# Performance work log

Hardware: AMD Instinct MI355X
Metric: run time of the kernel (lower is better)

The kernel has to match this reference:

```python
import math
import jax, jax.numpy as jnp
import numpy as np

H = 12
D_MODEL = 768
D_K = D_MODEL // H
B, S = 2, 2048


def setup_inputs() -> dict:
    key = jax.random.key(0)
    ks = jax.random.split(key, 12)
    sc = 0.02
    inp = {
        "query": jax.random.normal(ks[0], (B, S, D_MODEL), jnp.float32),
        "key": jax.random.normal(ks[1], (B, S, D_MODEL), jnp.float32),
        "value": jax.random.normal(ks[2], (B, S, D_MODEL), jnp.float32),
        # causal mask [B, S, S]: 1 where attendable
        "mask": jnp.broadcast_to(jnp.tril(jnp.ones((S, S), jnp.int32)), (B, S, S)),
        "Wq": sc * jax.random.normal(ks[3], (D_MODEL, D_MODEL), jnp.float32),
        "bq": jnp.zeros((D_MODEL,), jnp.float32),
        "Wk": sc * jax.random.normal(ks[4], (D_MODEL, D_MODEL), jnp.float32),
        "bk": jnp.zeros((D_MODEL,), jnp.float32),
        "Wv": sc * jax.random.normal(ks[5], (D_MODEL, D_MODEL), jnp.float32),
        "bv": jnp.zeros((D_MODEL,), jnp.float32),
        "Wo": sc * jax.random.normal(ks[6], (D_MODEL, D_MODEL), jnp.float32),
        "bo": jnp.zeros((D_MODEL,), jnp.float32),
    }
    return inp


def reference(query, key, value, mask, Wq, bq, Wk, bk, Wv, bv, Wo, bo):
    b, s, _ = query.shape
    # linear projections (torch Linear: x @ W.T + b), split into heads
    def proj(x, W, bias):
        return (x @ W.T + bias).reshape(b, s, H, D_K).transpose(0, 2, 1, 3)  # [B,H,S,Dk]

    q = proj(query, Wq, bq)
    k = proj(key, Wk, bk)
    v = proj(value, Wv, bv)

    scores = jnp.einsum("bhqd,bhkd->bhqk", q, k) / math.sqrt(D_K)  # [B,H,S,S]
    # exponential time-decay bias over key positions 1..S, shape [1,1,1,S]
    time = jnp.exp(-jnp.arange(1, s + 1, dtype=scores.dtype))[None, None, None, :]
    scores = jnp.where(mask[:, None, :, :] == 0, jnp.asarray(-1e9, scores.dtype), scores)
    p_attn = jax.nn.softmax(scores - time, axis=-1)
    x = jnp.einsum("bhqk,bhkd->bhqd", p_attn, v)  # [B,H,S,Dk]
    x = x.transpose(0, 2, 1, 3).reshape(b, s, H * D_K)
    return x @ Wo.T + bo
```

## Files before the change

### kernel.cpp

```cpp
#include <hip/hip_runtime.h>
#include <hip/hip_bf16.h>
#include <math.h>

typedef __bf16 bf16;
typedef __attribute__((ext_vector_type(8))) __bf16 bf16x8;
typedef __attribute__((ext_vector_type(4))) __bf16 bf16x4;
typedef __attribute__((ext_vector_type(4))) float floatx4;
typedef __attribute__((ext_vector_type(16))) float floatx16;

#define NH 12
#define DK 64
#define DM 768
#define NB 2
#define SEQ 2048
#define MTOT (NB * SEQ)
#define WELEM (DM * DM)
#define XELEM (MTOT * DM)

#define QSCALE 0.1803368801111832f
#define LOG2E 1.4426950408889634f

static __device__ __forceinline__ bf16x8 load8(const bf16* p) {
    return *(const bf16x8*)p;
}
static __device__ __forceinline__ float4 ld4(const float* p) {
    return *(const float4*)p;
}
static __device__ __forceinline__ bf16x8 cvt8(const float4 a, const float4 b) {
    bf16x8 r;
    r[0] = (bf16)a.x; r[1] = (bf16)a.y; r[2] = (bf16)a.z; r[3] = (bf16)a.w;
    r[4] = (bf16)b.x; r[5] = (bf16)b.y; r[6] = (bf16)b.z; r[7] = (bf16)b.w;
    return r;
}
static __device__ __forceinline__ float fast_exp2(float x) {
#if __has_builtin(__builtin_amdgcn_exp2f)
    return __builtin_amdgcn_exp2f(x);
#else
    return __expf(x * 0.6931471805599453f);
#endif
}
static __device__ __forceinline__ floatx16 zero16() {
    floatx16 z;
#pragma unroll
    for (int i = 0; i < 16; i++) z[i] = 0.f;
    return z;
}
static __device__ __forceinline__ void async16(const bf16* g, bf16* l) {
    __builtin_amdgcn_global_load_lds((const __attribute__((address_space(1))) void*)g,
                                     (__attribute__((address_space(3))) void*)l,
                                     16, 0, 0);
}

__global__ __launch_bounds__(256) void cvt_kernel(
    const float* __restrict__ wq, const float* __restrict__ wk,
    const float* __restrict__ wv, const float* __restrict__ wo,
    const float* __restrict__ xq, const float* __restrict__ xk, const float* __restrict__ xv,
    bf16* __restrict__ Wb, bf16* __restrict__ Wob,
    bf16* __restrict__ Xqb, bf16* __restrict__ Xkb, bf16* __restrict__ Xvb) {
    const int g = blockIdx.x * 256 + threadIdx.x;
    const int PW = WELEM / 8;
    const int PX = XELEM / 8;
    if (g < 4 * PW) {
        const int wi = g / PW;
        const int rem = g - wi * PW;
        const int n = rem / 96;
        const int t = rem - n * 96;
        const int s = t >> 3;
        const int j = t & 7;
        const float* src = (wi == 0) ? wq : (wi == 1) ? wk : (wi == 2) ? wv : wo;
        bf16* dst = (wi < 3) ? (Wb + (size_t)wi * WELEM) : Wob;
        const float* p = src + (size_t)n * DM + s * 64 + j * 8;
        *(bf16x8*)(dst + (size_t)n * DM + s * 64 + ((j ^ (n & 7)) * 8)) = cvt8(ld4(p), ld4(p + 4));
    } else {
        const int gx = g - 4 * PW;
        const int xi = gx / PX;
        const int rem = gx - xi * PX;
        const int m = rem / 96;
        const int t = rem - m * 96;
        const int s = t >> 3;
        const int j = t & 7;
        const float* src = (xi == 0) ? xq : (xi == 1) ? xk : xv;
        bf16* dst = (xi == 0) ? Xqb : (xi == 1) ? Xkb : Xvb;
        const float* p = src + (size_t)m * DM + s * 64 + j * 8;
        *(bf16x8*)(dst + (size_t)m * DM + s * 64 + ((j ^ (m & 7)) * 8)) = cvt8(ld4(p), ld4(p + 4));
    }
}

__global__ __launch_bounds__(256, 3) void qkv_kernel(
    const bf16* __restrict__ Xqb, const bf16* __restrict__ Xkb, const bf16* __restrict__ Xvb,
    const bf16* __restrict__ Wb,
    const float* __restrict__ bq, const float* __restrict__ bk, const float* __restrict__ bv,
    bf16* __restrict__ Oq, bf16* __restrict__ Ok, bf16* __restrict__ Ov) {
    __shared__ __align__(16) bf16 SM[2 * 64 * 64 + 2 * 128 * 64];
    bf16* As0 = SM;
    bf16* Bs0 = SM + 8192;

    const int tid = threadIdx.x;
    const int id = blockIdx.x;
    const int xcd = id & 7;
    const int sl = id >> 3;
    const int z = sl / 48;
    const int r = sl % 48;
    const int m0 = (xcd * 8 + r / 6) * 64;
    const int n0 = (r % 6) * 128;

    const bf16* X = (z == 0) ? Xqb : (z == 1) ? Xkb : Xvb;
    const bf16* W = Wb + (size_t)z * WELEM;
    const float* bias = (z == 0) ? bq : (z == 1) ? bk : bv;
    bf16* out = (z == 0) ? Oq : (z == 1) ? Ok : Ov;

    const int wv = tid >> 6;
    const int wm = wv >> 1, wn = wv & 1;
    const int lane = tid & 63;
    const int ln = lane & 15;
    const int kq = lane >> 4;
    const int drow = lane >> 3;
    const int dcol = (lane & 7) * 8;

    floatx4 acc[2][4];
#pragma unroll
    for (int i = 0; i < 2; i++)
#pragma unroll
        for (int j = 0; j < 4; j++) acc[i][j] = (floatx4){0.f, 0.f, 0.f, 0.f};

#pragma unroll
    for (int it = 0; it < 2; it++)
        async16(X + (size_t)(m0 + wv * 16 + it * 8 + drow) * DM + dcol,
                As0 + (wv * 16 + it * 8) * 64);
#pragma unroll
    for (int it = 0; it < 4; it++)
        async16(W + (size_t)(n0 + wv * 32 + it * 8 + drow) * DM + dcol,
                Bs0 + (wv * 32 + it * 8) * 64);

    for (int k = 0; k < 12; k++) {
        __syncthreads();
        const bf16* Ap = As0 + (k & 1) * 4096;
        const bf16* Bp = Bs0 + (k & 1) * 8192;
        if (k < 11) {
            const int kc = (k + 1) * 64;
            bf16* An = As0 + ((k + 1) & 1) * 4096;
            bf16* Bn = Bs0 + ((k + 1) & 1) * 8192;
#pragma unroll
            for (int it = 0; it < 2; it++)
                async16(X + (size_t)(m0 + wv * 16 + it * 8 + drow) * DM + kc + dcol,
                        An + (wv * 16 + it * 8) * 64);
#pragma unroll
            for (int it = 0; it < 4; it++)
                async16(W + (size_t)(n0 + wv * 32 + it * 8 + drow) * DM + kc + dcol,
                        Bn + (wv * 32 + it * 8) * 64);
        }
#pragma unroll
        for (int ks = 0; ks < 2; ks++) {
            const int jb = (ks * 4 + kq) ^ (ln & 7);
            bf16x8 af[2], bfm[4];
#pragma unroll
            for (int mt = 0; mt < 2; mt++)
                af[mt] = *(const bf16x8*)&Ap[(wm * 32 + mt * 16 + ln) * 64 + jb * 8];
#pragma unroll
            for (int nt = 0; nt < 4; nt++)
                bfm[nt] = *(const bf16x8*)&Bp[(wn * 64 + nt * 16 + ln) * 64 + jb * 8];
#pragma unroll
            for (int mt = 0; mt < 2; mt++)
#pragma unroll
                for (int nt = 0; nt < 4; nt++)
                    acc[mt][nt] = __builtin_amdgcn_mfma_f32_16x16x32_bf16(af[mt], bfm[nt], acc[mt][nt], 0, 0, 0);
        }
    }

    float bv4[4];
#pragma unroll
    for (int nt = 0; nt < 4; nt++) bv4[nt] = bias[n0 + wn * 64 + nt * 16 + ln];

    if (z < 2) {
        const float qs = (z == 0) ? QSCALE : 1.0f;
        __syncthreads();
        bf16 (*E)[136] = (bf16(*)[136])SM;
#pragma unroll
        for (int mt = 0; mt < 2; mt++)
#pragma unroll
            for (int nt = 0; nt < 4; nt++)
#pragma unroll
                for (int r2 = 0; r2 < 4; r2++)
                    E[wm * 32 + mt * 16 + kq * 4 + r2][wn * 64 + nt * 16 + ln] =
                        (bf16)((acc[mt][nt][r2] + bv4[nt]) * qs);
        __syncthreads();
        const int row = tid >> 2;
        const int cb = (tid & 3) * 32;
        const int m = m0 + row;
        const int b = m >> 11;
        const int s = m & (SEQ - 1);
        const int h = (n0 + cb) >> 6;
        const int d = (n0 + cb) & 63;
        bf16* op = &out[((size_t)(b * NH + h) * SEQ + s) * DK + d];
#pragma unroll
        for (int q2 = 0; q2 < 4; q2++)
            *(bf16x8*)(op + q2 * 8) = *(bf16x8*)&E[row][cb + q2 * 8];
    } else {
        __syncthreads();
        bf16 (*E)[72] = (bf16(*)[72])SM;
#pragma unroll
        for (int nt = 0; nt < 4; nt++)
#pragma unroll
            for (int mt = 0; mt < 2; mt++) {
                bf16x4 v;
#pragma unroll
                for (int r2 = 0; r2 < 4; r2++) v[r2] = (bf16)(acc[mt][nt][r2] + bv4[nt]);
                *(bf16x4*)&E[wn * 64 + nt * 16 + ln][wm * 32 + mt * 16 + kq * 4] = v;
            }
        __syncthreads();
        const int row = tid >> 1;
        const int sc = (tid & 1) * 32;
        const int b = m0 >> 11;
        const int s0 = m0 & (SEQ - 1);
        const int h = (n0 >> 6) + (row >> 6);
        const int d = row & 63;
        bf16* op = &out[(size_t)(b * NH + h) * DK * SEQ + (size_t)d * SEQ + s0 + sc];
#pragma unroll
        for (int q2 = 0; q2 < 4; q2++)
            *(bf16x8*)(op + q2 * 8) = *(bf16x8*)&E[row][sc + q2 * 8];
    }
}


#define PERMK(r) (((r) & ~12) | (((r) & 4) << 1) | (((r) & 8) >> 1))
#define VSWZ(g, d) (((g) & 8) | (((g) & 7) ^ ((d) & 7)))

#define STAGE(kc)                                                                   \
    {                                                                               \
        bf16* kb_ = SM + group * 16384;                                             \
        bf16* vb_ = kb_ + 8192;                                                     \
        const int kk0 = (kc) * 128;                                                 \
        _Pragma("unroll")                                                           \
        for (int it = 0; it < 4; it++) {                                            \
            const int sk = qw * 4 + it;                                             \
            const int rK = sk * 8 + (lane >> 3);                                    \
            const int jbK = lane & 7;                                               \
            async16(Kb + (size_t)(kk0 + PERMK(rK)) * DK + ((jbK ^ (rK & 7)) * 8),   \
                    kb_ + sk * 512);                                                \
            const int dV = sk * 4 + (lane >> 4);                                    \
            const int jbV = lane & 15;                                              \
            async16(Vb + (size_t)dV * SEQ + kk0 + (VSWZ(jbV, dV) * 8),              \
                    vb_ + sk * 512);                                                \
        }                                                                           \
    }

#define CHUNK_BODY(FIRSTC)                                                          \
    _Pragma("unroll")                                                               \
    for (int c2 = 0; c2 < 4; c2++) {                                                \
        const int rowk = c2 * 32 + ln32;                                            \
        const bf16* krow = Kc + rowk * 64;                                          \
        const int rs = rowk & 7;                                                    \
        const bf16x8 a0 = *(const bf16x8*)&krow[((0 + hi) ^ rs) * 8];               \
        const bf16x8 a1 = *(const bf16x8*)&krow[((2 + hi) ^ rs) * 8];               \
        const bf16x8 a2 = *(const bf16x8*)&krow[((4 + hi) ^ rs) * 8];               \
        const bf16x8 a3 = *(const bf16x8*)&krow[((6 + hi) ^ rs) * 8];               \
        floatx16 t = zero16();                                                      \
        __builtin_amdgcn_s_setprio(1);                                              \
        t = __builtin_amdgcn_mfma_f32_32x32x16_bf16(a0, qb0, t, 0, 0, 0);           \
        t = __builtin_amdgcn_mfma_f32_32x32x16_bf16(a1, qb1, t, 0, 0, 0);           \
        t = __builtin_amdgcn_mfma_f32_32x32x16_bf16(a2, qb2, t, 0, 0, 0);           \
        t = __builtin_amdgcn_mfma_f32_32x32x16_bf16(a3, qb3, t, 0, 0, 0);           \
        __builtin_amdgcn_s_setprio(0);                                              \
        bf16x8 pa0, pa1;                                                            \
        _Pragma("unroll")                                                           \
        for (int r = 0; r < 16; r++) {                                              \
            const int kg = k0 + c2 * 32 + ((r >> 3) << 4) + (hi << 3) + (r & 7);    \
            float sv = t[r];                                                        \
            if (FIRSTC) sv -= __expf(-(float)(kg + 1)) * LOG2E;                     \
            float pf = fast_exp2(sv);                                               \
            if (lastc && kg > qgl) pf = 0.f;                                        \
            lsum += pf;                                                             \
            if (r < 8) pa0[r] = (bf16)pf; else pa1[r & 7] = (bf16)pf;               \
        }                                                                           \
        __builtin_amdgcn_s_setprio(1);                                              \
        {                                                                           \
            const bf16* v0 = Vc + ln32 * 128;                                       \
            const bf16* v1 = Vc + (32 + ln32) * 128;                                \
            const int ds = ln32 & 7;                                                \
            bf16x8 vb;                                                              \
            vb = *(const bf16x8*)&v0[VSWZ(c2 * 4 + hi, ds) * 8];                    \
            Oacc0 = __builtin_amdgcn_mfma_f32_32x32x16_bf16(pa0, vb, Oacc0, 0, 0, 0); \
            vb = *(const bf16x8*)&v0[VSWZ(c2 * 4 + 2 + hi, ds) * 8];                \
            Oacc0 = __builtin_amdgcn_mfma_f32_32x32x16_bf16(pa1, vb, Oacc0, 0, 0, 0); \
            vb = *(const bf16x8*)&v1[VSWZ(c2 * 4 + hi, ds) * 8];                    \
            Oacc1 = __builtin_amdgcn_mfma_f32_32x32x16_bf16(pa0, vb, Oacc1, 0, 0, 0); \
            vb = *(const bf16x8*)&v1[VSWZ(c2 * 4 + 2 + hi, ds) * 8];                \
            Oacc1 = __builtin_amdgcn_mfma_f32_32x32x16_bf16(pa1, vb, Oacc1, 0, 0, 0); \
        }                                                                           \
        __builtin_amdgcn_s_setprio(0);                                              \
    }

__global__ __launch_bounds__(512) void attn_kernel(const bf16* __restrict__ Q,
                                                   const bf16* __restrict__ K,
                                                   const bf16* __restrict__ Vt,
                                                   bf16* __restrict__ Xout) {
    __shared__ __align__(16) bf16 SM[2 * 16384];

    const int tid = threadIdx.x;
    const int gw = tid >> 6;
    const int group = gw >> 2;
    const int qw = gw & 3;
    const int lane = tid & 63;
    const int ln32 = lane & 31;
    const int hi = lane >> 5;

    const int b0 = blockIdx.x;
    const int t = (b0 < 192) ? (15 - b0 / 24) : ((b0 - 192) / 24);
    const int bh = b0 % 24;

    const int q0 = t * 128;
    const int nch = t + 1;

    const bf16* Qb = Q + (size_t)bh * SEQ * DK;
    const bf16* Kb = K + (size_t)bh * SEQ * DK;
    const bf16* Vb = Vt + (size_t)bh * SEQ * DK;

    const int qrow = q0 + qw * 32 + ln32;
    const int qgl = qrow;

    const bf16x8 qb0 = load8(Qb + (size_t)qrow * DK + 0 + hi * 8);
    const bf16x8 qb1 = load8(Qb + (size_t)qrow * DK + 16 + hi * 8);
    const bf16x8 qb2 = load8(Qb + (size_t)qrow * DK + 32 + hi * 8);
    const bf16x8 qb3 = load8(Qb + (size_t)qrow * DK + 48 + hi * 8);

    float lsum = 0.f;
    floatx16 Oacc0 = zero16(), Oacc1 = zero16();

    const int R = (nch + 1) >> 1;
    for (int r = 0; r < R; r++) {
        const int c = 2 * r + group;
        const bool active = (c < nch);
        __syncthreads();
        if (active) STAGE(c)
        asm volatile("s_waitcnt vmcnt(0)" ::: "memory");
        __syncthreads();
        if (active) {
            const int k0 = c * 128;
            const bool lastc = (c == nch - 1);
            const bf16* Kc = SM + group * 16384;
            const bf16* Vc = Kc + 8192;
            if (c == 0) {
                CHUNK_BODY(true)
            } else {
                CHUNK_BODY(false)
            }
        }
    }

    lsum += __shfl_xor(lsum, 32, 64);

    __syncthreads();
    float* LF = (float*)SM;
    float* LS = (float*)SM + 128 * 68;
    if (group == 1) {
#pragma unroll
        for (int r = 0; r < 16; r++) {
            const int rq = (r & 3) + ((r >> 2) << 3) + (hi << 2);
            LF[(qw * 32 + rq) * 68 + ln32] = Oacc0[r];
            LF[(qw * 32 + rq) * 68 + 32 + ln32] = Oacc1[r];
        }
        if (hi == 0) LS[qw * 32 + ln32] = lsum;
    }
    __syncthreads();
    float inv = 0.f;
    if (group == 0) {
        lsum += LS[qw * 32 + ln32];
#pragma unroll
        for (int r = 0; r < 16; r++) {
            const int rq = (r & 3) + ((r >> 2) << 3) + (hi << 2);
            Oacc0[r] += LF[(qw * 32 + rq) * 68 + ln32];
            Oacc1[r] += LF[(qw * 32 + rq) * 68 + 32 + ln32];
        }
        inv = 1.f / lsum;
    }
    __syncthreads();

    bf16 (*E)[72] = (bf16(*)[72])SM;
    if (group == 0) {
#pragma unroll
        for (int r = 0; r < 16; r++) {
            const int rq = (r & 3) + ((r >> 2) << 3) + (hi << 2);
            const float rv = __shfl(inv, rq, 64);
            E[qw * 32 + rq][ln32] = (bf16)(Oacc0[r] * rv);
            E[qw * 32 + rq][32 + ln32] = (bf16)(Oacc1[r] * rv);
        }
    }
    __syncthreads();

    if (tid < 256) {
        const int b = bh / NH;
        const int h = bh - b * NH;
        const int row = tid >> 1;
        const int colh = (tid & 1) * 32;
        const int q = q0 + row;
        const int key = row & 7;
        bf16* rowp = &Xout[((size_t)(b * SEQ + q)) * DM + h * DK];
#pragma unroll
        for (int s2 = 0; s2 < 4; s2++) {
            const int jb = (tid & 1) * 4 + s2;
            *(bf16x8*)(rowp + ((jb ^ key) * 8)) = *(bf16x8*)&E[row][colh + s2 * 8];
        }
    }
}

__global__ __launch_bounds__(256, 3) void outproj_kernel(const bf16* __restrict__ X,
                                                         const bf16* __restrict__ W,
                                                         const float* __restrict__ bias,
                                                         float* __restrict__ out) {
    __shared__ __align__(16) bf16 SM[2 * 64 * 64 + 2 * 128 * 64];
    bf16* As0 = SM;
    bf16* Bs0 = SM + 8192;

    const int tid = threadIdx.x;
    const int id = blockIdx.x;
    const int xcd = id & 7;
    const int sl = id >> 3;
    const int m0 = (xcd * 8 + sl / 6) * 64;
    const int n0 = (sl % 6) * 128;

    const int wv = tid >> 6;
    const int wm = wv >> 1, wn = wv & 1;
    const int lane = tid & 63;
    const int ln = lane & 15;
    const int kq = lane >> 4;
    const int drow = lane >> 3;
    const int dcol = (lane & 7) * 8;

    floatx4 acc[2][4];
#pragma unroll
    for (int i = 0; i < 2; i++)
#pragma unroll
        for (int j = 0; j < 4; j++) acc[i][j] = (floatx4){0.f, 0.f, 0.f, 0.f};

#pragma unroll
    for (int it = 0; it < 2; it++)
        async16(X + (size_t)(m0 + wv * 16 + it * 8 + drow) * DM + dcol,
                As0 + (wv * 16 + it * 8) * 64);
#pragma unroll
    for (int it = 0; it < 4; it++)
        async16(W + (size_t)(n0 + wv * 32 + it * 8 + drow) * DM + dcol,
                Bs0 + (wv * 32 + it * 8) * 64);

    for (int k = 0; k < 12; k++) {
        __syncthreads();
        const bf16* Ap = As0 + (k & 1) * 4096;
        const bf16* Bp = Bs0 + (k & 1) * 8192;
        if (k < 11) {
            const int kc = (k + 1) * 64;
            bf16* An = As0 + ((k + 1) & 1) * 4096;
            bf16* Bn = Bs0 + ((k + 1) & 1) * 8192;
#pragma unroll
            for (int it = 0; it < 2; it++)
                async16(X + (size_t)(m0 + wv * 16 + it * 8 + drow) * DM + kc + dcol,
                        An + (wv * 16 + it * 8) * 64);
#pragma unroll
            for (int it = 0; it < 4; it++)
                async16(W + (size_t)(n0 + wv * 32 + it * 8 + drow) * DM + kc + dcol,
                        Bn + (wv * 32 + it * 8) * 64);
        }
#pragma unroll
        for (int ks = 0; ks < 2; ks++) {
            const int jb = (ks * 4 + kq) ^ (ln & 7);
            bf16x8 af[2], bfm[4];
#pragma unroll
            for (int mt = 0; mt < 2; mt++)
                af[mt] = *(const bf16x8*)&Ap[(wm * 32 + mt * 16 + ln) * 64 + jb * 8];
#pragma unroll
            for (int nt = 0; nt < 4; nt++)
                bfm[nt] = *(const bf16x8*)&Bp[(wn * 64 + nt * 16 + ln) * 64 + jb * 8];
#pragma unroll
            for (int mt = 0; mt < 2; mt++)
#pragma unroll
                for (int nt = 0; nt < 4; nt++)
                    acc[mt][nt] = __builtin_amdgcn_mfma_f32_16x16x32_bf16(af[mt], bfm[nt], acc[mt][nt], 0, 0, 0);
        }
    }

#pragma unroll
    for (int nt = 0; nt < 4; nt++) {
        const int n = n0 + wn * 64 + nt * 16 + ln;
        const float bval = bias[n];
#pragma unroll
        for (int mt = 0; mt < 2; mt++)
#pragma unroll
            for (int r2 = 0; r2 < 4; r2++) {
                const int m = m0 + wm * 32 + mt * 16 + kq * 4 + r2;
                out[(size_t)m * DM + n] = acc[mt][nt][r2] + bval;
            }
    }
}

extern "C" void kernel_launch(void* const* d_in, const int* in_sizes, int n_in,
                              void* d_out, int out_size, void* d_ws, size_t ws_size,
                              hipStream_t stream) {
    const float* query = (const float*)d_in[0];
    const float* key   = (const float*)d_in[1];
    const float* value = (const float*)d_in[2];
    const float* Wq = (const float*)d_in[4];
    const float* bq = (const float*)d_in[5];
    const float* Wk = (const float*)d_in[6];
    const float* bk = (const float*)d_in[7];
    const float* Wv = (const float*)d_in[8];
    const float* bv = (const float*)d_in[9];
    const float* Wo = (const float*)d_in[10];
    const float* bo = (const float*)d_in[11];
    float* out = (float*)d_out;

    bf16* Qws  = (bf16*)d_ws;
    bf16* Kws  = Qws + XELEM;
    bf16* Vtws = Kws + XELEM;
    bf16* Xws  = Vtws + XELEM;
    bf16* Wob  = Xws + XELEM;
    bf16* Xvb  = Wob + WELEM;

    bf16* Wb  = (bf16*)out;
    bf16* Xkb = (bf16*)out + 3 * WELEM;

    bf16* Xqb = Xws;

    const int ncvt = (4 * (WELEM / 8) + 3 * (XELEM / 8)) / 256;
    cvt_kernel<<<ncvt, 256, 0, stream>>>(Wq, Wk, Wv, Wo, query, key, value,
                                         Wb, Wob, Xqb, Xkb, Xvb);

    qkv_kernel<<<1152, 256, 0, stream>>>(Xqb, Xkb, Xvb, Wb, bq, bk, bv,
                                         Qws, Kws, Vtws);

    attn_kernel<<<384, 512, 0, stream>>>(Qws, Kws, Vtws, Xws);

    outproj_kernel<<<384, 256, 0, stream>>>(Xws, Wob, bo, out);
}
```

Measured before the change: 194.9 us.

## Double-buffer attention K/V chunks and split each chunk across wave groups

The attention loop previously had the two wave groups take alternating 128-key chunks, with no prefetch: each round staged a chunk and waited for it before computing. Now all 8 waves stage each chunk cooperatively into one of two shared-memory buffers, prefetch chunk c+1 while computing chunk c, and each group handles its own 64-key half of every chunk. Separate instantiations for the last chunk remove the causal-mask compare from interior chunks. This adds a second barrier per chunk and splits the same number of MFMAs into smaller per-chunk pieces.

```diff
diff --git a/kernel.cpp b/kernel.cpp
--- a/kernel.cpp
+++ b/kernel.cpp
@@ -44,6 +44,9 @@
 #pragma unroll
     for (int i = 0; i < 16; i++) z[i] = 0.f;
     return z;
+}
+static __device__ __forceinline__ floatx16 mfma32(bf16x8 a, bf16x8 b, floatx16 c) {
+    return __builtin_amdgcn_mfma_f32_32x32x16_bf16(a, b, c, 0, 0, 0);
 }
 static __device__ __forceinline__ void async16(const bf16* g, bf16* l) {
     __builtin_amdgcn_global_load_lds((const __attribute__((address_space(1))) void*)g,
@@ -225,29 +228,34 @@
 #define PERMK(r) (((r) & ~12) | (((r) & 4) << 1) | (((r) & 8) >> 1))
 #define VSWZ(g, d) (((g) & 8) | (((g) & 7) ^ ((d) & 7)))
 
-#define STAGE(kc)                                                                   \
+#define STAGE(kc, bsel)                                                             \
     {                                                                               \
-        bf16* kb_ = SM + group * 16384;                                             \
+        bf16* kb_ = SM + (bsel) * 16384;                                            \
         bf16* vb_ = kb_ + 8192;                                                     \
         const int kk0 = (kc) * 128;                                                 \
         _Pragma("unroll")                                                           \
         for (int it = 0; it < 4; it++) {                                            \
-            const int sk = qw * 4 + it;                                             \
-            const int rK = sk * 8 + (lane >> 3);                                    \
-            const int jbK = lane & 7;                                               \
-            async16(Kb + (size_t)(kk0 + PERMK(rK)) * DK + ((jbK ^ (rK & 7)) * 8),   \
-                    kb_ + sk * 512);                                                \
-            const int dV = sk * 4 + (lane >> 4);                                    \
-            const int jbV = lane & 15;                                              \
-            async16(Vb + (size_t)dV * SEQ + kk0 + (VSWZ(jbV, dV) * 8),              \
-                    vb_ + sk * 512);                                                \
+            const int sk = gw * 4 + it;                                             \
+            if (sk < 16) {                                                          \
+                const int rK = sk * 8 + (lane >> 3);                                \
+                const int jbK = lane & 7;                                           \
+                async16(Kb + (size_t)(kk0 + PERMK(rK)) * DK + ((jbK ^ (rK & 7)) * 8), \
+                        kb_ + sk * 512);                                            \
+            } else {                                                                \
+                const int sv = sk - 16;                                             \
+                const int dV = sv * 4 + (lane >> 4);                                \
+                const int jbV = lane & 15;                                          \
+                async16(Vb + (size_t)dV * SEQ + kk0 + (VSWZ(jbV, dV) * 8),          \
+                        vb_ + sv * 512);                                            \
+            }                                                                       \
         }                                                                           \
     }
 
-#define CHUNK_BODY(FIRSTC)                                                          \
+#define CHUNK_BODY(FIRSTC, LASTC)                                                   \
     _Pragma("unroll")                                                               \
-    for (int c2 = 0; c2 < 4; c2++) {                                                \
-        const int rowk = c2 * 32 + ln32;                                            \
+    for (int c2 = 0; c2 < 2; c2++) {                                                \
+        const int kb = g64 + c2 * 32;                                               \
+        const int rowk = kb + ln32;                                                 \
         const bf16* krow = Kc + rowk * 64;                                          \
         const int rs = rowk & 7;                                                    \
         const bf16x8 a0 = *(const bf16x8*)&krow[((0 + hi) ^ rs) * 8];               \
@@ -256,19 +264,24 @@
         const bf16x8 a3 = *(const bf16x8*)&krow[((6 + hi) ^ rs) * 8];               \
         floatx16 t = zero16();                                                      \
         __builtin_amdgcn_s_setprio(1);                                              \
-        t = __builtin_amdgcn_mfma_f32_32x32x16_bf16(a0, qb0, t, 0, 0, 0);           \
-        t = __builtin_amdgcn_mfma_f32_32x32x16_bf16(a1, qb1, t, 0, 0, 0);           \
-        t = __builtin_amdgcn_mfma_f32_32x32x16_bf16(a2, qb2, t, 0, 0, 0);           \
-        t = __builtin_amdgcn_mfma_f32_32x32x16_bf16(a3, qb3, t, 0, 0, 0);           \
+        t = mfma32(a0, qb0, t);                                                     \
+        t = mfma32(a1, qb1, t);                                                     \
+        t = mfma32(a2, qb2, t);                                                     \
+        t = mfma32(a3, qb3, t);                                                     \
         __builtin_amdgcn_s_setprio(0);                                              \
         bf16x8 pa0, pa1;                                                            \
         _Pragma("unroll")                                                           \
         for (int r = 0; r < 16; r++) {                                              \
-            const int kg = k0 + c2 * 32 + ((r >> 3) << 4) + (hi << 3) + (r & 7);    \
             float sv = t[r];                                                        \
-            if (FIRSTC) sv -= __expf(-(float)(kg + 1)) * LOG2E;                     \
+            if (FIRSTC) {                                                           \
+                const int kg = k0 + kb + ((r >> 3) << 4) + (hi << 3) + (r & 7);     \
+                sv -= __expf(-(float)(kg + 1)) * LOG2E;                             \
+            }                                                                       \
             float pf = fast_exp2(sv);                                               \
-            if (lastc && kg > qgl) pf = 0.f;                                        \
+            if (LASTC) {                                                            \
+                const int kg = k0 + kb + ((r >> 3) << 4) + (hi << 3) + (r & 7);     \
+                if (kg > qgl) pf = 0.f;                                             \
+            }                                                                       \
             lsum += pf;                                                             \
             if (r < 8) pa0[r] = (bf16)pf; else pa1[r & 7] = (bf16)pf;               \
         }                                                                           \
@@ -277,15 +290,16 @@
             const bf16* v0 = Vc + ln32 * 128;                                       \
             const bf16* v1 = Vc + (32 + ln32) * 128;                                \
             const int ds = ln32 & 7;                                                \
+            const int gb = (g64 >> 3) + c2 * 4;                                     \
             bf16x8 vb;                                                              \
-            vb = *(const bf16x8*)&v0[VSWZ(c2 * 4 + hi, ds) * 8];                    \
-            Oacc0 = __builtin_amdgcn_mfma_f32_32x32x16_bf16(pa0, vb, Oacc0, 0, 0, 0); \
-            vb = *(const bf16x8*)&v0[VSWZ(c2 * 4 + 2 + hi, ds) * 8];                \
-            Oacc0 = __builtin_amdgcn_mfma_f32_32x32x16_bf16(pa1, vb, Oacc0, 0, 0, 0); \
-            vb = *(const bf16x8*)&v1[VSWZ(c2 * 4 + hi, ds) * 8];                    \
-            Oacc1 = __builtin_amdgcn_mfma_f32_32x32x16_bf16(pa0, vb, Oacc1, 0, 0, 0); \
-            vb = *(const bf16x8*)&v1[VSWZ(c2 * 4 + 2 + hi, ds) * 8];                \
-            Oacc1 = __builtin_amdgcn_mfma_f32_32x32x16_bf16(pa1, vb, Oacc1, 0, 0, 0); \
+            vb = *(const bf16x8*)&v0[VSWZ(gb + hi, ds) * 8];                        \
+            Oacc0 = mfma32(pa0, vb, Oacc0);                                         \
+            vb = *(const bf16x8*)&v0[VSWZ(gb + 2 + hi, ds) * 8];                    \
+            Oacc0 = mfma32(pa1, vb, Oacc0);                                         \
+            vb = *(const bf16x8*)&v1[VSWZ(gb + hi, ds) * 8];                        \
+            Oacc1 = mfma32(pa0, vb, Oacc1);                                         \
+            vb = *(const bf16x8*)&v1[VSWZ(gb + 2 + hi, ds) * 8];                    \
+            Oacc1 = mfma32(pa1, vb, Oacc1);                                         \
         }                                                                           \
         __builtin_amdgcn_s_setprio(0);                                              \
     }
@@ -298,8 +312,9 @@
 
     const int tid = threadIdx.x;
     const int gw = tid >> 6;
-    const int group = gw >> 2;
+    const int g = gw >> 2;
     const int qw = gw & 3;
+    const int g64 = g * 64;
     const int lane = tid & 63;
     const int ln32 = lane & 31;
     const int hi = lane >> 5;
@@ -326,25 +341,29 @@
     float lsum = 0.f;
     floatx16 Oacc0 = zero16(), Oacc1 = zero16();
 
-    const int R = (nch + 1) >> 1;
-    for (int r = 0; r < R; r++) {
-        const int c = 2 * r + group;
-        const bool active = (c < nch);
-        __syncthreads();
-        if (active) STAGE(c)
-        asm volatile("s_waitcnt vmcnt(0)" ::: "memory");
-        __syncthreads();
-        if (active) {
-            const int k0 = c * 128;
-            const bool lastc = (c == nch - 1);
-            const bf16* Kc = SM + group * 16384;
-            const bf16* Vc = Kc + 8192;
-            if (c == 0) {
-                CHUNK_BODY(true)
-            } else {
-                CHUNK_BODY(false)
-            }
-        }
+    STAGE(0, 0)
+
+    for (int c = 0; c < nch; c++) {
+        if (c + 1 < nch) {
+            STAGE(c + 1, (c + 1) & 1)
+            asm volatile("s_waitcnt vmcnt(4)" ::: "memory");
+        } else {
+            asm volatile("s_waitcnt vmcnt(0)" ::: "memory");
+        }
+        __syncthreads();
+        const bf16* Kc = SM + (c & 1) * 16384;
+        const bf16* Vc = Kc + 8192;
+        const int k0 = c * 128;
+        const bool lastc = (c == nch - 1);
+        if (c == 0) {
+            if (lastc) { CHUNK_BODY(true, true) }
+            else       { CHUNK_BODY(true, false) }
+        } else if (lastc) {
+            CHUNK_BODY(false, true)
+        } else {
+            CHUNK_BODY(false, false)
+        }
+        __syncthreads();
     }
 
     lsum += __shfl_xor(lsum, 32, 64);
@@ -352,7 +371,7 @@
     __syncthreads();
     float* LF = (float*)SM;
     float* LS = (float*)SM + 128 * 68;
-    if (group == 1) {
+    if (g == 1) {
 #pragma unroll
         for (int r = 0; r < 16; r++) {
             const int rq = (r & 3) + ((r >> 2) << 3) + (hi << 2);
@@ -363,7 +382,7 @@
     }
     __syncthreads();
     float inv = 0.f;
-    if (group == 0) {
+    if (g == 0) {
         lsum += LS[qw * 32 + ln32];
 #pragma unroll
         for (int r = 0; r < 16; r++) {
@@ -376,7 +395,7 @@
     __syncthreads();
 
     bf16 (*E)[72] = (bf16(*)[72])SM;
-    if (group == 0) {
+    if (g == 0) {
 #pragma unroll
         for (int r = 0; r < 16; r++) {
             const int rq = (r & 3) + ((r >> 2) << 3) + (hi << 2);
```

Result: no change. 191.3 us (-1.8%).
